# Kernel tuning notes

Hardware: AMD Instinct MI355X
Metric: run time of the kernel (lower is better)

Reference implementation:

```python
import jax, jax.numpy as jnp
import numpy as np

NEG_INF = -jnp.inf


def _rope(x, cos, sin):
    # x: (B, S, H, D); cos/sin: (1, S, 1, D//2)
    xr = x.reshape(*x.shape[:-1], -1, 2)
    x1, x2 = xr[..., 0], xr[..., 1]  # (B, S, H, D//2) each
    # faithful to source: concat halves along last axis, same total size D
    return jnp.concatenate([x1 * cos - x2 * sin, x1 * sin + x2 * cos], axis=-1)


def setup_inputs() -> dict:
    B, S, D, H, Ld = 2, 2048, 2048, 16, 128
    key = jax.random.key(0)
    ks = jax.random.split(key, 6)
    sc = 1.0 / np.sqrt(D)
    return {
        "x": jax.random.normal(ks[0], (B, S, D), jnp.float32),
        "attn_mask": jnp.ones((B, S), jnp.int32),
        "Wq": jax.random.normal(ks[1], (D, H * Ld), jnp.float32) * sc,
        "bq": jnp.zeros((H * Ld,), jnp.float32),
        "Wk": jax.random.normal(ks[2], (D, H * Ld), jnp.float32) * sc,
        "bk": jnp.zeros((H * Ld,), jnp.float32),
        "Wv": jax.random.normal(ks[3], (D, H * Ld), jnp.float32) * sc,
        "bv": jnp.zeros((H * Ld,), jnp.float32),
        "Wo": jax.random.normal(ks[4], (H * Ld, D), jnp.float32) * sc,
        "bo": jnp.zeros((D,), jnp.float32),
        "num_heads": H,
    }


def reference(x, attn_mask, Wq, bq, Wk, bk, Wv, bv, Wo, bo, num_heads):
    B, S, D = x.shape
    H = int(num_heads)
    Ld = Wq.shape[1] // H
    base = 10000

    q = (x @ Wq + bq).reshape(B, S, H, Ld)
    k = (x @ Wk + bk).reshape(B, S, H, Ld)
    v = (x @ Wv + bv).reshape(B, S, H, Ld)

    # rotary tables (match RotaryEmbedding.setup, sliced to seq_len)
    inv_freq = 1.0 / base ** (2 * jnp.arange(0, Ld // 2) / Ld)
    angles = jnp.arange(S)[:, None] * inv_freq[None, :]  # (S, Ld//2)
    cos = jnp.cos(angles)[None, :, None, :].astype(x.dtype)
    sin = jnp.sin(angles)[None, :, None, :].astype(x.dtype)
    q = _rope(q, cos, sin)
    k = _rope(k, cos, sin)

    q = jnp.transpose(q, (0, 2, 1, 3))  # (B, H, S, Ld)
    k = jnp.transpose(k, (0, 2, 1, 3))
    v = jnp.transpose(v, (0, 2, 1, 3))

    scale = jnp.sqrt(jnp.float32(Ld)).astype(x.dtype)
    scores = jnp.einsum('bnqd,bnkd->bnqk', q, k) / scale  # (B, H, S, S)

    # faithful mask from source: keep where arange[None,:] >= arange[:,None]
    row_idx = jnp.arange(S)[None, :]
    col_idx = jnp.arange(S)[:, None]
    keep = row_idx >= col_idx  # (S, S)
    scores = jnp.where(keep[None, None, :, :], scores, NEG_INF)

    # padding mask applied over the QUERY axis, as in source: (B,1,S,1)
    scores = jnp.where(attn_mask[:, None, :, None] > 0, scores, NEG_INF)

    attn = jax.nn.softmax(scores, axis=-1)
    attended = jnp.einsum('bnqk,bnkd->bnqd', attn, v)
    attended = jnp.transpose(attended, (0, 2, 1, 3)).reshape(B, S, H * Ld)
    return attended @ Wo + bo
```

## Files before the change

kernel.cpp:

```cpp
#include <hip/hip_runtime.h>
#include <math.h>

typedef __bf16 bf16x8 __attribute__((ext_vector_type(8)));
typedef float f32x4 __attribute__((ext_vector_type(4)));

#define MFMA_BF16(a,b,c) __builtin_amdgcn_mfma_f32_16x16x32_bf16((a),(b),(c),0,0,0)

static constexpr int S_LEN = 2048;
static constexpr int DM    = 2048;
static constexpr int NHEAD = 16;
static constexpr int LDH   = 128;
static constexpr int BATCH = 2;
static constexpr size_t QKV_SEG = (size_t)BATCH * NHEAD * S_LEN * LDH;

__device__ __forceinline__ unsigned short f2bf(float f) {
    unsigned u = __float_as_uint(f);
    u += 0x7fffu + ((u >> 16) & 1u);
    return (unsigned short)(u >> 16);
}
__device__ __forceinline__ float bf2f(unsigned short h) {
    return __uint_as_float(((unsigned)h) << 16);
}
__device__ __forceinline__ float fexp2(float x) { return exp2f(x); }

__device__ __forceinline__ void ld_lds16(const void* g, void* l) {
    __builtin_amdgcn_global_load_lds(
        (const __attribute__((address_space(1))) unsigned int*)g,
        (__attribute__((address_space(3))) unsigned int*)l, 16, 0, 0);
}

__global__ void prep_all(const float* __restrict__ x, unsigned short* __restrict__ xb,
                         float* __restrict__ ct, float* __restrict__ st,
                         const float* __restrict__ W0, const float* __restrict__ W1,
                         const float* __restrict__ W2, const float* __restrict__ W3,
                         unsigned short* __restrict__ O0, unsigned short* __restrict__ O1,
                         unsigned short* __restrict__ O2, unsigned short* __restrict__ O3) {
    __shared__ unsigned short tile[32][33];
    int bid = blockIdx.x;
    int t = threadIdx.x;
    if (bid < 8192) {
        int idx = bid * 256 + t;
        float4 v = reinterpret_cast<const float4*>(x)[idx];
        unsigned lo = (unsigned)f2bf(v.x) | ((unsigned)f2bf(v.y) << 16);
        unsigned hi = (unsigned)f2bf(v.z) | ((unsigned)f2bf(v.w) << 16);
        reinterpret_cast<uint2*>(xb)[idx] = make_uint2(lo, hi);
    } else if (bid < 8704) {
        int i = t & 63;
        int s = (bid - 8192) * 4 + (t >> 6);
        float freq = (float)exp(-(double)(2 * i) / 128.0 * 9.210340371976184);
        float a = (float)s * freq;
        ct[s * 64 + i] = cosf(a);
        st[s * 64 + i] = sinf(a);
    } else {
        int wid = bid - 8704;
        int z = wid >> 12;
        int rem = wid & 4095;
        int k0 = (rem >> 6) * 32;
        int n0 = (rem & 63) * 32;
        const float* W = (z == 0) ? W0 : (z == 1) ? W1 : (z == 2) ? W2 : W3;
        unsigned short* Wt = (z == 0) ? O0 : (z == 1) ? O1 : (z == 2) ? O2 : O3;
        int ir = t >> 3, ic = (t & 7) * 4;
        float4 v = *reinterpret_cast<const float4*>(&W[(size_t)(k0 + ir) * DM + n0 + ic]);
        tile[ir][ic + 0] = f2bf(v.x);
        tile[ir][ic + 1] = f2bf(v.y);
        tile[ir][ic + 2] = f2bf(v.z);
        tile[ir][ic + 3] = f2bf(v.w);
        __syncthreads();
        unsigned lo = (unsigned)tile[ic + 0][ir] | ((unsigned)tile[ic + 1][ir] << 16);
        unsigned hi = (unsigned)tile[ic + 2][ir] | ((unsigned)tile[ic + 3][ir] << 16);
        *reinterpret_cast<uint2*>(&Wt[(size_t)(n0 + ir) * DM + k0 + ic]) = make_uint2(lo, hi);
    }
}

__global__ __launch_bounds__(256, 2) void gemm_out_v2(
    const unsigned short* __restrict__ A,
    const unsigned short* __restrict__ Bt,
    const float* __restrict__ b0,
    float* __restrict__ outp)
{
    constexpr int K  = DM;
    constexpr int NT = K / 32;
    constexpr int SLOT_B = 24576;
    __shared__ __attribute__((aligned(16))) unsigned short smem[36864];

    int t = threadIdx.x, lane = t & 63, w = t >> 6;
    int i16 = lane & 15, quad = lane >> 4;
    int wc = w & 1, wr = w >> 1;

    int flat = blockIdx.y * 16 + blockIdx.x;
    int xcd = flat & 7, r8 = flat >> 3;
    int nbx = xcd * 2 + (r8 >> 4);
    int nby = r8 & 15;
    int m0 = nby * 256, n0 = nbx * 128;

    const unsigned short* ga[4];
    const unsigned short* gb[2];
    int loffA[4], loffB[2];
#pragma unroll
    for (int j = 0; j < 4; ++j) {
        int off = j * 4096 + t * 16;
        int row = off >> 6;
        int g = ((off >> 4) & 3) ^ ((row >> 1) & 3);
        ga[j] = A + (size_t)(m0 + row) * K + g * 8;
        loffA[j] = off;
    }
#pragma unroll
    for (int j = 0; j < 2; ++j) {
        int off = j * 4096 + t * 16;
        int row = off >> 6;
        int g = ((off >> 4) & 3) ^ ((row >> 1) & 3);
        gb[j] = Bt + (size_t)(n0 + row) * K + g * 8;
        loffB[j] = off;
    }

    auto stage = [&](int slot, int kt) {
        char* base = (char*)smem + slot * SLOT_B;
#pragma unroll
        for (int j = 0; j < 4; ++j)
            ld_lds16(ga[j] + kt * 32, base + loffA[j]);
#pragma unroll
        for (int j = 0; j < 2; ++j)
            ld_lds16(gb[j] + kt * 32, base + 16384 + loffB[j]);
    };

    f32x4 acc[8][4];
    const f32x4 z4 = {0.f, 0.f, 0.f, 0.f};
#pragma unroll
    for (int mi = 0; mi < 8; ++mi)
#pragma unroll
        for (int ni = 0; ni < 4; ++ni) acc[mi][ni] = z4;

    auto compute = [&](int slot) {
        const char* Ab = (const char*)smem + slot * SLOT_B;
        const char* Bb = Ab + 16384;
        bf16x8 bF[4];
#pragma unroll
        for (int ni = 0; ni < 4; ++ni) {
            int rB = wc * 64 + ni * 16 + i16;
            bF[ni] = *reinterpret_cast<const bf16x8*>(
                Bb + rB * 64 + ((quad ^ ((rB >> 1) & 3)) * 16));
        }
#pragma unroll
        for (int h = 0; h < 2; ++h) {
            bf16x8 aF[4];
#pragma unroll
            for (int mi = 0; mi < 4; ++mi) {
                int rA = wr * 128 + h * 64 + mi * 16 + i16;
                aF[mi] = *reinterpret_cast<const bf16x8*>(
                    Ab + rA * 64 + ((quad ^ ((rA >> 1) & 3)) * 16));
            }
            __builtin_amdgcn_s_setprio(1);
#pragma unroll
            for (int mi = 0; mi < 4; ++mi)
#pragma unroll
                for (int ni = 0; ni < 4; ++ni)
                    acc[h * 4 + mi][ni] = MFMA_BF16(aF[mi], bF[ni], acc[h * 4 + mi][ni]);
            __builtin_amdgcn_s_setprio(0);
        }
    };

    stage(0, 0); stage(1, 1);
    asm volatile("s_waitcnt vmcnt(6)" ::: "memory");
    __builtin_amdgcn_s_barrier();
    asm volatile("" ::: "memory");

    int cs = 0, ssl = 2;
    for (int tt = 0; tt < NT - 2; ++tt) {
        stage(ssl, tt + 2);
        compute(cs);
        asm volatile("s_waitcnt vmcnt(6)" ::: "memory");
        __builtin_amdgcn_s_barrier();
        asm volatile("" ::: "memory");
        cs  = (cs  == 2) ? 0 : cs  + 1;
        ssl = (ssl == 2) ? 0 : ssl + 1;
    }
    compute(cs);
    asm volatile("s_waitcnt vmcnt(0)" ::: "memory");
    __builtin_amdgcn_s_barrier();
    asm volatile("" ::: "memory");
    cs = (cs == 2) ? 0 : cs + 1;
    compute(cs);

#pragma unroll
    for (int mi = 0; mi < 8; ++mi)
#pragma unroll
        for (int ni = 0; ni < 4; ++ni) {
            int nn = n0 + wc * 64 + ni * 16 + i16;
            float bv = b0[nn];
#pragma unroll
            for (int r = 0; r < 4; ++r) {
                int mm = m0 + wr * 128 + mi * 16 + quad * 4 + r;
                outp[(size_t)mm * DM + nn] = acc[mi][ni][r] + bv;
            }
        }
}

__global__ __launch_bounds__(256, 2) void gemm_qkv_v2(
    const unsigned short* __restrict__ A,
    const unsigned short* __restrict__ Bt,
    const float* __restrict__ b0, const float* __restrict__ b1,
    const float* __restrict__ b2,
    const float* __restrict__ ctab, const float* __restrict__ stab,
    unsigned short* __restrict__ outp)
{
    constexpr int K  = DM;
    constexpr int NT = K / 32;
    constexpr int SLOT_B = 24576;
    __shared__ __attribute__((aligned(16))) unsigned short smem[36864];

    int t = threadIdx.x, lane = t & 63, w = t >> 6;
    int i16 = lane & 15, quad = lane >> 4;
    int wc = w & 1, wr = w >> 1;

    int flat = blockIdx.y * 48 + blockIdx.x;
    int xcd = flat & 7, r8 = flat >> 3;
    int nbx = xcd * 6 + (r8 >> 4);
    int nby = r8 & 15;
    int m0 = nby * 256, n0 = nbx * 128;

    const unsigned short* ga[4];
    const unsigned short* gb[2];
    int loffA[4], loffB[2];
#pragma unroll
    for (int j = 0; j < 4; ++j) {
        int off = j * 4096 + t * 16;
        int row = off >> 6;
        int g = ((off >> 4) & 3) ^ ((row >> 1) & 3);
        ga[j] = A + (size_t)(m0 + row) * K + g * 8;
        loffA[j] = off;
    }
#pragma unroll
    for (int j = 0; j < 2; ++j) {
        int off = j * 4096 + t * 16;
        int row = off >> 6;
        int g = ((off >> 4) & 3) ^ ((row >> 1) & 3);
        gb[j] = Bt + (size_t)(n0 + row) * K + g * 8;
        loffB[j] = off;
    }

    auto stage = [&](int slot, int kt) {
        char* base = (char*)smem + slot * SLOT_B;
#pragma unroll
        for (int j = 0; j < 4; ++j)
            ld_lds16(ga[j] + kt * 32, base + loffA[j]);
#pragma unroll
        for (int j = 0; j < 2; ++j)
            ld_lds16(gb[j] + kt * 32, base + 16384 + loffB[j]);
    };

    f32x4 acc[8][4];
    const f32x4 z4 = {0.f, 0.f, 0.f, 0.f};
#pragma unroll
    for (int mi = 0; mi < 8; ++mi)
#pragma unroll
        for (int ni = 0; ni < 4; ++ni) acc[mi][ni] = z4;

    auto compute = [&](int slot) {
        const char* Ab = (const char*)smem + slot * SLOT_B;
        const char* Bb = Ab + 16384;
        bf16x8 bF[4];
#pragma unroll
        for (int ni = 0; ni < 4; ++ni) {
            int rB = wc * 64 + ni * 16 + i16;
            bF[ni] = *reinterpret_cast<const bf16x8*>(
                Bb + rB * 64 + ((quad ^ ((rB >> 1) & 3)) * 16));
        }
#pragma unroll
        for (int h = 0; h < 2; ++h) {
            bf16x8 aF[4];
#pragma unroll
            for (int mi = 0; mi < 4; ++mi) {
                int rA = wr * 128 + h * 64 + mi * 16 + i16;
                aF[mi] = *reinterpret_cast<const bf16x8*>(
                    Ab + rA * 64 + ((quad ^ ((rA >> 1) & 3)) * 16));
            }
            __builtin_amdgcn_s_setprio(1);
#pragma unroll
            for (int mi = 0; mi < 4; ++mi)
#pragma unroll
                for (int ni = 0; ni < 4; ++ni)
                    acc[h * 4 + mi][ni] = MFMA_BF16(aF[mi], bF[ni], acc[h * 4 + mi][ni]);
            __builtin_amdgcn_s_setprio(0);
        }
    };

    stage(0, 0); stage(1, 1);
    asm volatile("s_waitcnt vmcnt(6)" ::: "memory");
    __builtin_amdgcn_s_barrier();
    asm volatile("" ::: "memory");

    int cs = 0, ssl = 2;
    for (int tt = 0; tt < NT - 2; ++tt) {
        stage(ssl, tt + 2);
        compute(cs);
        asm volatile("s_waitcnt vmcnt(6)" ::: "memory");
        __builtin_amdgcn_s_barrier();
        asm volatile("" ::: "memory");
        cs  = (cs  == 2) ? 0 : cs  + 1;
        ssl = (ssl == 2) ? 0 : ssl + 1;
    }
    compute(cs);
    asm volatile("s_waitcnt vmcnt(0)" ::: "memory");
    __builtin_amdgcn_s_barrier();
    asm volatile("" ::: "memory");
    cs = (cs == 2) ? 0 : cs + 1;
    compute(cs);
    __syncthreads();

    unsigned short* Cs = smem;
    int which = n0 >> 11;
    int hh = (n0 & 2047) >> 7;
    const float* bp = (which == 0) ? b0 : ((which == 1) ? b1 : b2);
    int segn = n0 & 2047;
    int bb = m0 >> 11, s0 = m0 & 2047;

    if (which == 2) {
#pragma unroll
        for (int mi = 0; mi < 8; ++mi)
#pragma unroll
            for (int ni = 0; ni < 4; ++ni) {
                int d = wc * 64 + ni * 16 + i16;
                float bv = bp[segn + d];
#pragma unroll
                for (int r = 0; r < 4; ++r) {
                    int sl = wr * 128 + mi * 16 + quad * 4 + r;
                    Cs[d * 256 + (((sl >> 3) ^ (d & 31)) * 8) + (sl & 7)] =
                        f2bf(acc[mi][ni][r] + bv);
                }
            }
        __syncthreads();
        unsigned short* vout = outp + 2 * QKV_SEG;
#pragma unroll
        for (int it = 0; it < 16; ++it) {
            int idx = it * 256 + t;
            int d = idx >> 5, sg = idx & 31;
            uint4 v = *reinterpret_cast<const uint4*>(
                &Cs[d * 256 + ((sg ^ (d & 31)) * 8)]);
            size_t oidx = (((size_t)(bb * NHEAD + hh)) * LDH + d) * S_LEN + s0 + sg * 8;
            *reinterpret_cast<uint4*>(vout + oidx) = v;
        }
    } else {
#pragma unroll
        for (int mi = 0; mi < 8; ++mi)
#pragma unroll
            for (int ni = 0; ni < 4; ++ni) {
                int nl = wc * 64 + ni * 16 + i16;
                float bv = bp[segn + nl];
#pragma unroll
                for (int r = 0; r < 4; ++r) {
                    int ml = wr * 128 + mi * 16 + quad * 4 + r;
                    Cs[ml * 128 + nl] = f2bf(acc[mi][ni][r] + bv);
                }
            }
        __syncthreads();
        float qscale = (which == 0) ? (0.08838834764831845f * 1.4426950408889634f) : 1.0f;
        unsigned short* qout = outp + (size_t)which * QKV_SEG;
#pragma unroll
        for (int it = 0; it < 16; ++it) {
            int idx = it * 256 + t;
            int row = idx >> 4, c16 = idx & 15;
            int mm = m0 + row;
            int ss = mm & 2047, bb2 = mm >> 11;
            int i8 = (c16 & 7) * 8;
            const unsigned short* crow = Cs + row * 128 + i8 * 2;
            uint4 w0 = *reinterpret_cast<const uint4*>(crow);
            uint4 w1 = *reinterpret_cast<const uint4*>(crow + 8);
            unsigned pw[8] = {w0.x, w0.y, w0.z, w0.w, w1.x, w1.y, w1.z, w1.w};
            float4 cA = *reinterpret_cast<const float4*>(&ctab[ss * 64 + i8]);
            float4 cB = *reinterpret_cast<const float4*>(&ctab[ss * 64 + i8 + 4]);
            float4 sA = *reinterpret_cast<const float4*>(&stab[ss * 64 + i8]);
            float4 sB = *reinterpret_cast<const float4*>(&stab[ss * 64 + i8 + 4]);
            float cv[8] = {cA.x, cA.y, cA.z, cA.w, cB.x, cB.y, cB.z, cB.w};
            float sv[8] = {sA.x, sA.y, sA.z, sA.w, sB.x, sB.y, sB.z, sB.w};
            bool hi = (c16 >= 8);
            unsigned short ov[8];
#pragma unroll
            for (int j = 0; j < 8; ++j) {
                float xe = bf2f((unsigned short)(pw[j] & 0xffff));
                float xo = bf2f((unsigned short)(pw[j] >> 16));
                float o = hi ? (xe * sv[j] + xo * cv[j]) : (xe * cv[j] - xo * sv[j]);
                ov[j] = f2bf(o * qscale);
            }
            size_t oidx = (((size_t)(bb2 * NHEAD + hh)) * S_LEN + ss) * LDH + c16 * 8;
            *reinterpret_cast<uint4*>(qout + oidx) =
                *reinterpret_cast<const uint4*>(ov);
        }
    }
}

__global__ __launch_bounds__(256, 3) void attn_kernel(
    const unsigned short* __restrict__ q,
    const unsigned short* __restrict__ k,
    const unsigned short* __restrict__ vt,
    unsigned short* __restrict__ att)
{
    __shared__ __attribute__((aligned(16))) unsigned short Ks[2][32 * 128];
    __shared__ __attribute__((aligned(16))) unsigned short Vs[2][128 * 32];
    __shared__ __attribute__((aligned(16))) unsigned short Ps[4][32 * 32];

    int bid = blockIdx.x;
    int second = bid >> 8;
    int p = bid & 255;
    int xb = second ? (15 - (p >> 5)) : (p >> 5);
    int bh = p & 31;
    int b = bh >> 4, h = bh & (NHEAD - 1);
    int q0 = xb * 128;

    int t = threadIdx.x, w = t >> 6, lane = t & 63;
    int i16 = lane & 15, quad = lane >> 4;
    int qbase = q0 + w * 32;

    bf16x8 qf[2][4];
#pragma unroll
    for (int qs = 0; qs < 2; ++qs) {
        const unsigned short* qrow = q + ((size_t)bh * S_LEN + qbase + qs * 16 + i16) * LDH;
#pragma unroll
        for (int c = 0; c < 4; ++c)
            qf[qs][c] = *reinterpret_cast<const bf16x8*>(qrow + c * 32 + quad * 8);
    }

    const f32x4 z4 = {0.f, 0.f, 0.f, 0.f};
    f32x4 o[2][8];
#pragma unroll
    for (int qs = 0; qs < 2; ++qs)
#pragma unroll
        for (int dt = 0; dt < 8; ++dt) o[qs][dt] = z4;
    float l_i[2] = {0.f, 0.f};

    const unsigned short* kbh  = k  + (size_t)bh * S_LEN * LDH;
    const unsigned short* vtbh = vt + (size_t)bh * LDH * S_LEN;
    unsigned short* PsW = Ps[w];

    auto stage = [&](int buf, int kk0) {
#pragma unroll
        for (int j = 0; j < 2; ++j) {
            int off = j * 4096 + t * 16;
            int key = off >> 8;
            int gk = ((off >> 4) & 15) ^ (key & 15);
            ld_lds16(&kbh[(size_t)(kk0 + key) * LDH + gk * 8], (char*)Ks[buf] + off);
            int d = off >> 6;
            int gv = ((off >> 4) & 3) ^ (d & 3);
            ld_lds16(&vtbh[(size_t)d * S_LEN + kk0 + gv * 8], (char*)Vs[buf] + off);
        }
    };

    stage(0, q0);
    int nch = (S_LEN - q0) >> 5;
    for (int ci = 0; ci < nch; ++ci) {
        __syncthreads();
        if (ci + 1 < nch) stage((ci + 1) & 1, q0 + (ci + 1) * 32);
        int kk0 = q0 + ci * 32;
        if (kk0 + 32 <= qbase) continue;
        const unsigned short* Kb = Ks[ci & 1];
        const unsigned short* Vb = Vs[ci & 1];

        f32x4 s[2][2];
#pragma unroll
        for (int qs = 0; qs < 2; ++qs)
#pragma unroll
            for (int kn = 0; kn < 2; ++kn) s[qs][kn] = z4;
#pragma unroll
        for (int c = 0; c < 4; ++c) {
            bf16x8 kf[2];
#pragma unroll
            for (int kn = 0; kn < 2; ++kn) {
                int key = kn * 16 + i16;
                int gs = (c * 4 + quad) ^ (key & 15);
                kf[kn] = *reinterpret_cast<const bf16x8*>((const char*)Kb + key * 256 + gs * 16);
            }
            __builtin_amdgcn_s_setprio(1);
#pragma unroll
            for (int qs = 0; qs < 2; ++qs)
#pragma unroll
                for (int kn = 0; kn < 2; ++kn)
                    s[qs][kn] = MFMA_BF16(kf[kn], qf[qs][c], s[qs][kn]);
            __builtin_amdgcn_s_setprio(0);
        }

        bool diag = (kk0 == qbase);
#pragma unroll
        for (int qs = 0; qs < 2; ++qs) {
            int q_local = qs * 16 + i16;
            int qg = qbase + q_local;
#pragma unroll
            for (int kn = 0; kn < 2; ++kn) {
                int keyb = kk0 + kn * 16 + quad * 4;
                float pv[4];
                if (diag) {
#pragma unroll
                    for (int r = 0; r < 4; ++r)
                        pv[r] = (keyb + r >= qg) ? fexp2(s[qs][kn][r]) : 0.f;
                } else {
#pragma unroll
                    for (int r = 0; r < 4; ++r) pv[r] = fexp2(s[qs][kn][r]);
                }
                l_i[qs] += (pv[0] + pv[1]) + (pv[2] + pv[3]);
                unsigned lo = (unsigned)f2bf(pv[0]) | ((unsigned)f2bf(pv[1]) << 16);
                unsigned hi = (unsigned)f2bf(pv[2]) | ((unsigned)f2bf(pv[3]) << 16);
                int g = (kn * 2 + (quad >> 1)) ^ (q_local & 3);
                char* addr = (char*)PsW + q_local * 64 + g * 16 + (quad & 1) * 8;
                *reinterpret_cast<uint2*>(addr) = make_uint2(lo, hi);
            }
        }

        bf16x8 pf[2];
#pragma unroll
        for (int qs = 0; qs < 2; ++qs) {
            int q_local = qs * 16 + i16;
            int g = quad ^ (q_local & 3);
            pf[qs] = *reinterpret_cast<const bf16x8*>((const char*)PsW + q_local * 64 + g * 16);
        }
        __builtin_amdgcn_s_setprio(1);
#pragma unroll
        for (int dt = 0; dt < 8; ++dt) {
            int d = dt * 16 + i16;
            int gv = quad ^ (d & 3);
            bf16x8 vf = *reinterpret_cast<const bf16x8*>((const char*)Vb + d * 64 + gv * 16);
            o[0][dt] = MFMA_BF16(pf[0], vf, o[0][dt]);
            o[1][dt] = MFMA_BF16(pf[1], vf, o[1][dt]);
        }
        __builtin_amdgcn_s_setprio(0);
    }

#pragma unroll
    for (int qs = 0; qs < 2; ++qs) {
        float lr = l_i[qs];
        lr += __shfl_xor(lr, 16);
        lr += __shfl_xor(lr, 32);
        l_i[qs] = lr;
    }
#pragma unroll
    for (int qs = 0; qs < 2; ++qs) {
#pragma unroll
        for (int r = 0; r < 4; ++r) {
            float lv = __shfl(l_i[qs], quad * 4 + r);
            float inv = 1.0f / lv;
            int qrow = qbase + qs * 16 + quad * 4 + r;
            unsigned short* orow = att + ((size_t)b * S_LEN + qrow) * DM + h * LDH;
#pragma unroll
            for (int dt = 0; dt < 8; ++dt)
                orow[dt * 16 + i16] = f2bf(o[qs][dt][r] * inv);
        }
    }
}

extern "C" void kernel_launch(void* const* d_in, const int* in_sizes, int n_in,
                              void* d_out, int out_size, void* d_ws, size_t ws_size,
                              hipStream_t stream) {
    const float* x  = (const float*)d_in[0];
    const float* Wq = (const float*)d_in[2];
    const float* bq = (const float*)d_in[3];
    const float* Wk = (const float*)d_in[4];
    const float* bk = (const float*)d_in[5];
    const float* Wv = (const float*)d_in[6];
    const float* bv = (const float*)d_in[7];
    const float* Wo = (const float*)d_in[8];
    const float* bo = (const float*)d_in[9];

    char* ws = (char*)d_ws;
    unsigned short* xb  = (unsigned short*)(ws);
    unsigned short* Wqt = (unsigned short*)(ws + 16777216);
    unsigned short* Wkt = (unsigned short*)(ws + 25165824);
    unsigned short* Wvt = (unsigned short*)(ws + 33554432);
    unsigned short* Wot = (unsigned short*)(ws + 41943040);
    unsigned short* qkv = (unsigned short*)(ws + 50331648);
    unsigned short* att = (unsigned short*)(ws + 100663296);
    float* ctab = (float*)(ws + 117440512);
    float* stab = (float*)(ws + 117964800);

    prep_all<<<25088, 256, 0, stream>>>(x, xb, ctab, stab,
                                        Wq, Wk, Wv, Wo, Wqt, Wkt, Wvt, Wot);

    gemm_qkv_v2<<<dim3(48, 16), 256, 0, stream>>>(
        xb, Wqt, bq, bk, bv, ctab, stab, qkv);

    attn_kernel<<<512, 256, 0, stream>>>(qkv, qkv + QKV_SEG, qkv + 2 * QKV_SEG, att);

    gemm_out_v2<<<dim3(16, 16), 256, 0, stream>>>(att, Wot, bo, (float*)d_out);
}
```

Before: 390.5 us.

## Cut QKV GEMM shared memory to double buffering and split epilogue for three blocks per CU

The QKV projection GEMM moves from a three-slot to a two-slot LDS ring, with an extra barrier between compute and the next stage load. The epilogue is split into two passes, one per warp row, so the staging buffer fits in the smaller LDS allocation. Launch bounds rise from 2 to 3 blocks per CU to raise occupancy. In exchange, each k-step now has an extra barrier, load/compute overlap is reduced, and register pressure is tighter, which could cause spills.

```diff
diff --git a/kernel.cpp b/kernel.cpp
--- a/kernel.cpp
+++ b/kernel.cpp
@@ -195,7 +195,7 @@
         }
 }
 
-__global__ __launch_bounds__(256, 2) void gemm_qkv_v2(
+__global__ __launch_bounds__(256, 3) void gemm_qkv_v3(
     const unsigned short* __restrict__ A,
     const unsigned short* __restrict__ Bt,
     const float* __restrict__ b0, const float* __restrict__ b1,
@@ -206,7 +206,7 @@
     constexpr int K  = DM;
     constexpr int NT = K / 32;
     constexpr int SLOT_B = 24576;
-    __shared__ __attribute__((aligned(16))) unsigned short smem[36864];
+    __shared__ __attribute__((aligned(16))) unsigned short smem[24576];
 
     int t = threadIdx.x, lane = t & 63, w = t >> 6;
     int i16 = lane & 15, quad = lane >> 4;
@@ -289,22 +289,20 @@
     __builtin_amdgcn_s_barrier();
     asm volatile("" ::: "memory");
 
-    int cs = 0, ssl = 2;
     for (int tt = 0; tt < NT - 2; ++tt) {
-        stage(ssl, tt + 2);
-        compute(cs);
+        compute(tt & 1);
+        __builtin_amdgcn_s_barrier();
+        asm volatile("" ::: "memory");
+        stage(tt & 1, tt + 2);
         asm volatile("s_waitcnt vmcnt(6)" ::: "memory");
         __builtin_amdgcn_s_barrier();
         asm volatile("" ::: "memory");
-        cs  = (cs  == 2) ? 0 : cs  + 1;
-        ssl = (ssl == 2) ? 0 : ssl + 1;
-    }
-    compute(cs);
+    }
+    compute((NT - 2) & 1);
     asm volatile("s_waitcnt vmcnt(0)" ::: "memory");
     __builtin_amdgcn_s_barrier();
     asm volatile("" ::: "memory");
-    cs = (cs == 2) ? 0 : cs + 1;
-    compute(cs);
+    compute((NT - 1) & 1);
     __syncthreads();
 
     unsigned short* Cs = smem;
@@ -315,75 +313,88 @@
     int bb = m0 >> 11, s0 = m0 & 2047;
 
     if (which == 2) {
-#pragma unroll
-        for (int mi = 0; mi < 8; ++mi)
-#pragma unroll
-            for (int ni = 0; ni < 4; ++ni) {
-                int d = wc * 64 + ni * 16 + i16;
-                float bv = bp[segn + d];
-#pragma unroll
-                for (int r = 0; r < 4; ++r) {
-                    int sl = wr * 128 + mi * 16 + quad * 4 + r;
-                    Cs[d * 256 + (((sl >> 3) ^ (d & 31)) * 8) + (sl & 7)] =
-                        f2bf(acc[mi][ni][r] + bv);
-                }
-            }
-        __syncthreads();
         unsigned short* vout = outp + 2 * QKV_SEG;
 #pragma unroll
-        for (int it = 0; it < 16; ++it) {
-            int idx = it * 256 + t;
-            int d = idx >> 5, sg = idx & 31;
-            uint4 v = *reinterpret_cast<const uint4*>(
-                &Cs[d * 256 + ((sg ^ (d & 31)) * 8)]);
-            size_t oidx = (((size_t)(bb * NHEAD + hh)) * LDH + d) * S_LEN + s0 + sg * 8;
-            *reinterpret_cast<uint4*>(vout + oidx) = v;
+        for (int p = 0; p < 2; ++p) {
+            if (wr == p) {
+#pragma unroll
+                for (int mi = 0; mi < 8; ++mi)
+#pragma unroll
+                    for (int ni = 0; ni < 4; ++ni) {
+                        int d = wc * 64 + ni * 16 + i16;
+                        float bv = bp[segn + d];
+#pragma unroll
+                        for (int r = 0; r < 4; ++r) {
+                            int sl = mi * 16 + quad * 4 + r;
+                            Cs[d * 128 + (((sl >> 3) ^ (d & 15)) * 8) + (sl & 7)] =
+                                f2bf(acc[mi][ni][r] + bv);
+                        }
+                    }
+            }
+            __syncthreads();
+#pragma unroll
+            for (int it = 0; it < 8; ++it) {
+                int idx = it * 256 + t;
+                int d = idx >> 4, sg = idx & 15;
+                uint4 v = *reinterpret_cast<const uint4*>(
+                    &Cs[d * 128 + ((sg ^ (d & 15)) * 8)]);
+                size_t oidx = (((size_t)(bb * NHEAD + hh)) * LDH + d) * S_LEN
+                              + s0 + p * 128 + sg * 8;
+                *reinterpret_cast<uint4*>(vout + oidx) = v;
+            }
+            __syncthreads();
         }
     } else {
-#pragma unroll
-        for (int mi = 0; mi < 8; ++mi)
-#pragma unroll
-            for (int ni = 0; ni < 4; ++ni) {
-                int nl = wc * 64 + ni * 16 + i16;
-                float bv = bp[segn + nl];
-#pragma unroll
-                for (int r = 0; r < 4; ++r) {
-                    int ml = wr * 128 + mi * 16 + quad * 4 + r;
-                    Cs[ml * 128 + nl] = f2bf(acc[mi][ni][r] + bv);
-                }
-            }
-        __syncthreads();
         float qscale = (which == 0) ? (0.08838834764831845f * 1.4426950408889634f) : 1.0f;
         unsigned short* qout = outp + (size_t)which * QKV_SEG;
 #pragma unroll
-        for (int it = 0; it < 16; ++it) {
-            int idx = it * 256 + t;
-            int row = idx >> 4, c16 = idx & 15;
-            int mm = m0 + row;
-            int ss = mm & 2047, bb2 = mm >> 11;
-            int i8 = (c16 & 7) * 8;
-            const unsigned short* crow = Cs + row * 128 + i8 * 2;
-            uint4 w0 = *reinterpret_cast<const uint4*>(crow);
-            uint4 w1 = *reinterpret_cast<const uint4*>(crow + 8);
-            unsigned pw[8] = {w0.x, w0.y, w0.z, w0.w, w1.x, w1.y, w1.z, w1.w};
-            float4 cA = *reinterpret_cast<const float4*>(&ctab[ss * 64 + i8]);
-            float4 cB = *reinterpret_cast<const float4*>(&ctab[ss * 64 + i8 + 4]);
-            float4 sA = *reinterpret_cast<const float4*>(&stab[ss * 64 + i8]);
-            float4 sB = *reinterpret_cast<const float4*>(&stab[ss * 64 + i8 + 4]);
-            float cv[8] = {cA.x, cA.y, cA.z, cA.w, cB.x, cB.y, cB.z, cB.w};
-            float sv[8] = {sA.x, sA.y, sA.z, sA.w, sB.x, sB.y, sB.z, sB.w};
-            bool hi = (c16 >= 8);
-            unsigned short ov[8];
-#pragma unroll
-            for (int j = 0; j < 8; ++j) {
-                float xe = bf2f((unsigned short)(pw[j] & 0xffff));
-                float xo = bf2f((unsigned short)(pw[j] >> 16));
-                float o = hi ? (xe * sv[j] + xo * cv[j]) : (xe * cv[j] - xo * sv[j]);
-                ov[j] = f2bf(o * qscale);
-            }
-            size_t oidx = (((size_t)(bb2 * NHEAD + hh)) * S_LEN + ss) * LDH + c16 * 8;
-            *reinterpret_cast<uint4*>(qout + oidx) =
-                *reinterpret_cast<const uint4*>(ov);
+        for (int p = 0; p < 2; ++p) {
+            if (wr == p) {
+#pragma unroll
+                for (int mi = 0; mi < 8; ++mi)
+#pragma unroll
+                    for (int ni = 0; ni < 4; ++ni) {
+                        int nl = wc * 64 + ni * 16 + i16;
+                        float bv = bp[segn + nl];
+#pragma unroll
+                        for (int r = 0; r < 4; ++r) {
+                            int ml = mi * 16 + quad * 4 + r;
+                            Cs[ml * 128 + nl] = f2bf(acc[mi][ni][r] + bv);
+                        }
+                    }
+            }
+            __syncthreads();
+#pragma unroll
+            for (int it = 0; it < 8; ++it) {
+                int idx = it * 256 + t;
+                int row = idx >> 4, c16 = idx & 15;
+                int mm = m0 + p * 128 + row;
+                int ss = mm & 2047, bb2 = mm >> 11;
+                int i8 = (c16 & 7) * 8;
+                const unsigned short* crow = Cs + row * 128 + i8 * 2;
+                uint4 w0 = *reinterpret_cast<const uint4*>(crow);
+                uint4 w1 = *reinterpret_cast<const uint4*>(crow + 8);
+                unsigned pw[8] = {w0.x, w0.y, w0.z, w0.w, w1.x, w1.y, w1.z, w1.w};
+                float4 cA = *reinterpret_cast<const float4*>(&ctab[ss * 64 + i8]);
+                float4 cB = *reinterpret_cast<const float4*>(&ctab[ss * 64 + i8 + 4]);
+                float4 sA = *reinterpret_cast<const float4*>(&stab[ss * 64 + i8]);
+                float4 sB = *reinterpret_cast<const float4*>(&stab[ss * 64 + i8 + 4]);
+                float cv[8] = {cA.x, cA.y, cA.z, cA.w, cB.x, cB.y, cB.z, cB.w};
+                float sv[8] = {sA.x, sA.y, sA.z, sA.w, sB.x, sB.y, sB.z, sB.w};
+                bool hi = (c16 >= 8);
+                unsigned short ov[8];
+#pragma unroll
+                for (int j = 0; j < 8; ++j) {
+                    float xe = bf2f((unsigned short)(pw[j] & 0xffff));
+                    float xo = bf2f((unsigned short)(pw[j] >> 16));
+                    float o = hi ? (xe * sv[j] + xo * cv[j]) : (xe * cv[j] - xo * sv[j]);
+                    ov[j] = f2bf(o * qscale);
+                }
+                size_t oidx = (((size_t)(bb2 * NHEAD + hh)) * S_LEN + ss) * LDH + c16 * 8;
+                *reinterpret_cast<uint4*>(qout + oidx) =
+                    *reinterpret_cast<const uint4*>(ov);
+            }
+            __syncthreads();
         }
     }
 }
@@ -571,7 +582,7 @@
     prep_all<<<25088, 256, 0, stream>>>(x, xb, ctab, stab,
                                         Wq, Wk, Wv, Wo, Wqt, Wkt, Wvt, Wot);
 
-    gemm_qkv_v2<<<dim3(48, 16), 256, 0, stream>>>(
+    gemm_qkv_v3<<<dim3(48, 16), 256, 0, stream>>>(
         xb, Wqt, bq, bk, bv, ctab, stab, qkv);
 
     attn_kernel<<<512, 256, 0, stream>>>(qkv, qkv + QKV_SEG, qkv + 2 * QKV_SEG, att);
```

Result: slower. 558.4 us (+43.0%).
